# Performance work log

Measured on AMD Instinct MI355X. Metric: run time of the kernel, lower is better.

## Reference

```python
import jax, jax.numpy as jnp
import numpy as np
import math

B, S, D, H, L, F = 32, 512, 512, 8, 4, 1024
TD = 4 * D  # time embedding dim
DH = D // H
SCALE = 1.0 / math.sqrt(DH)


def _ln(x, g, b):
    m = jnp.mean(x, -1, keepdims=True)
    v = jnp.var(x, -1, keepdims=True)
    return (x - m) * jax.lax.rsqrt(v + 1e-5) * g + b


def setup_inputs() -> dict:
    key = jax.random.key(0)
    ks = jax.random.split(key, 12)
    w = lambda k, shp: jax.random.normal(k, shp, dtype=jnp.float32) * 0.02
    return {
        "x": jax.random.normal(ks[0], (B, S, D), dtype=jnp.float32),
        "time": jax.random.uniform(ks[1], (B,), dtype=jnp.float32) * 1000.0,
        "time_w1": w(ks[2], (TD, D)), "time_b1": jnp.zeros((TD,), jnp.float32),
        "time_w2": w(ks[3], (TD, TD)), "time_b2": jnp.zeros((TD,), jnp.float32),
        "Wq": w(ks[4], (L, D, D)), "bq": jnp.zeros((L, D), jnp.float32),
        "Wk": w(ks[5], (L, D, D)), "bk": jnp.zeros((L, D), jnp.float32),
        "Wv": w(ks[6], (L, D, D)), "bv": jnp.zeros((L, D), jnp.float32),
        "Wo": w(ks[7], (L, D, D)), "bo": jnp.zeros((L, D), jnp.float32),
        "attn_g": jnp.ones((L, D), jnp.float32), "attn_b": jnp.zeros((L, D), jnp.float32),
        "ffn_g": jnp.ones((L, D), jnp.float32), "ffn_b": jnp.zeros((L, D), jnp.float32),
        "W1": w(ks[8], (L, 2 * F, D)), "b1": jnp.zeros((L, 2 * F), jnp.float32),
        "W2": w(ks[9], (L, D, F)), "b2": jnp.zeros((L, D), jnp.float32),
        "Wt": w(ks[10], (L, 4 * F, TD)), "bt": jnp.zeros((L, 4 * F), jnp.float32),
        "head_g": jnp.ones((D,), jnp.float32), "head_b": jnp.zeros((D,), jnp.float32),
        "Wh": w(ks[11], (D, D)), "bh": jnp.zeros((D,), jnp.float32),
    }


def _forward(x, time, time_w1, time_b1, time_w2, time_b2,
             Wq, bq, Wk, bk, Wv, bv, Wo, bo,
             attn_g, attn_b, ffn_g, ffn_b,
             W1, b1, W2, b2, Wt, bt,
             head_g, head_b, Wh, bh):
    Bsz = x.shape[0]
    # --- sinusoidal time embedding + time MLP ---
    half = D // 2
    freqs = jnp.exp(jnp.arange(half, dtype=jnp.float32) * (-math.log(10000.0) / (half - 1)))
    e = time[:, None] * freqs[None, :]
    temb = jnp.concatenate([jnp.sin(e), jnp.cos(e)], axis=-1)  # [B, D]
    temb = jax.nn.gelu(temb @ time_w1.T + time_b1, approximate=False) @ time_w2.T + time_b2  # [B, 4D]
    for i in range(L):
        # attention (prenorm; block 0 skips the norm since first_prenormalization=False)
        h = x if i == 0 else _ln(x, attn_g[i], attn_b[i])
        q = (h @ Wq[i].T + bq[i]).reshape(Bsz, S, H, DH)
        k = (h @ Wk[i].T + bk[i]).reshape(Bsz, S, H, DH)
        v = (h @ Wv[i].T + bv[i]).reshape(Bsz, S, H, DH)
        logits = jnp.einsum('bqhd,bkhd->bhqk', q, k) * SCALE
        probs = jax.nn.softmax(logits, axis=-1)
        o = jnp.einsum('bhqk,bkhd->bqhd', probs, v).reshape(Bsz, S, D)
        x = x + (o @ Wo[i].T + bo[i])
        # FFN with FiLM time conditioning and ReGLU activation
        h = _ln(x, ffn_g[i], ffn_b[i])
        h1 = h @ W1[i].T + b1[i]  # [B, S, 2F]
        tm = jax.nn.silu(temb) @ Wt[i].T + bt[i]  # [B, 4F]
        scale, shift = jnp.split(tm[:, None, :], 2, axis=-1)  # each [B, 1, 2F]
        h1 = h1 * (scale + 1.0) + shift
        a, g = jnp.split(h1, 2, axis=-1)  # ReGLU: a * relu(g)
        x = x + ((a * jax.nn.relu(g)) @ W2[i].T + b2[i])
    # head: last token -> LayerNorm -> ReLU -> Linear
    z = _ln(x[:, -1], head_g, head_b)
    return jax.nn.relu(z) @ Wh.T + bh


def reference(x, time, time_w1, time_b1, time_w2, time_b2,
              Wq, bq, Wk, bk, Wv, bv, Wo, bo,
              attn_g, attn_b, ffn_g, ffn_b,
              W1, b1, W2, b2, Wt, bt,
              head_g, head_b, Wh, bh):
    return _forward(x, time, time_w1, time_b1, time_w2, time_b2,
                    Wq, bq, Wk, bk, Wv, bv, Wo, bo,
                    attn_g, attn_b, ffn_g, ffn_b,
                    W1, b1, W2, b2, Wt, bt,
                    head_g, head_b, Wh, bh)
```

## Files before the change

### kernel.cpp

```cpp
#include <hip/hip_runtime.h>
#include <math.h>

typedef __bf16 bf16_t;
typedef __bf16 bf16x8 __attribute__((ext_vector_type(8)));
typedef float f32x4 __attribute__((ext_vector_type(4)));

__device__ __forceinline__ void gload_lds16(const void* g, void* l) {
    __builtin_amdgcn_global_load_lds(
        (const __attribute__((address_space(1))) void*)g,
        (__attribute__((address_space(3))) void*)l, 16, 0, 0);
}

__global__ void k_f2b(const float* __restrict__ in, bf16_t* __restrict__ out, int n8) {
    int idx = blockIdx.x * 256 + threadIdx.x;
    if (idx >= n8) return;
    const float* p = in + (size_t)idx * 8;
    bf16x8 r;
#pragma unroll
    for (int j = 0; j < 8; j++) r[j] = (bf16_t)p[j];
    *(bf16x8*)(out + (size_t)idx * 8) = r;
}

__global__ void k_time_embed(const float* __restrict__ time, float* __restrict__ temb0) {
    int b = blockIdx.x;
    int j = threadIdx.x;
    float f = __expf((float)j * -0.036118981458730134f);
    float e = time[b] * f;
    temb0[(size_t)b * 512 + j] = sinf(e);
    temb0[(size_t)b * 512 + 256 + j] = cosf(e);
}

template<bool DO_NORM>
__global__ void k_ln(const float* __restrict__ x, const float* __restrict__ g,
                     const float* __restrict__ b, bf16_t* __restrict__ out) {
    int row = blockIdx.x * 4 + (threadIdx.x >> 6);
    int lane = threadIdx.x & 63;
    const float* xr = x + (size_t)row * 512 + lane * 8;
    float4 v0 = *(const float4*)xr;
    float4 v1 = *(const float4*)(xr + 4);
    float vals[8] = {v0.x, v0.y, v0.z, v0.w, v1.x, v1.y, v1.z, v1.w};
    bf16x8 r;
    if (DO_NORM) {
        float s = 0.f, sq = 0.f;
#pragma unroll
        for (int j = 0; j < 8; j++) { s += vals[j]; sq += vals[j] * vals[j]; }
#pragma unroll
        for (int m = 1; m < 64; m <<= 1) { s += __shfl_xor(s, m, 64); sq += __shfl_xor(sq, m, 64); }
        float mean = s * (1.0f / 512.0f);
        float var = sq * (1.0f / 512.0f) - mean * mean;
        float rstd = rsqrtf(var + 1e-5f);
        float4 g0 = *(const float4*)(g + lane * 8);
        float4 g1 = *(const float4*)(g + lane * 8 + 4);
        float4 b0 = *(const float4*)(b + lane * 8);
        float4 b1 = *(const float4*)(b + lane * 8 + 4);
        float gs[8] = {g0.x, g0.y, g0.z, g0.w, g1.x, g1.y, g1.z, g1.w};
        float bs[8] = {b0.x, b0.y, b0.z, b0.w, b1.x, b1.y, b1.z, b1.w};
#pragma unroll
        for (int j = 0; j < 8; j++) r[j] = (bf16_t)((vals[j] - mean) * rstd * gs[j] + bs[j]);
    } else {
#pragma unroll
        for (int j = 0; j < 8; j++) r[j] = (bf16_t)vals[j];
    }
    *(bf16x8*)(out + (size_t)row * 512 + lane * 8) = r;
}

__global__ void k_head_prep(const float* __restrict__ x, const float* __restrict__ g,
                            const float* __restrict__ b, float* __restrict__ z) {
    int row = blockIdx.x * 4 + (threadIdx.x >> 6);
    int lane = threadIdx.x & 63;
    const float* xr = x + ((size_t)row * 512 + 511) * 512 + lane * 8;
    float4 v0 = *(const float4*)xr;
    float4 v1 = *(const float4*)(xr + 4);
    float vals[8] = {v0.x, v0.y, v0.z, v0.w, v1.x, v1.y, v1.z, v1.w};
    float s = 0.f, sq = 0.f;
#pragma unroll
    for (int j = 0; j < 8; j++) { s += vals[j]; sq += vals[j] * vals[j]; }
#pragma unroll
    for (int m = 1; m < 64; m <<= 1) { s += __shfl_xor(s, m, 64); sq += __shfl_xor(sq, m, 64); }
    float mean = s * (1.0f / 512.0f);
    float var = sq * (1.0f / 512.0f) - mean * mean;
    float rstd = rsqrtf(var + 1e-5f);
    float o[8];
#pragma unroll
    for (int j = 0; j < 8; j++) {
        float gv = g[lane * 8 + j], bv = b[lane * 8 + j];
        o[j] = fmaxf((vals[j] - mean) * rstd * gv + bv, 0.0f);
    }
    float* zr = z + (size_t)row * 512 + lane * 8;
    *(float4*)zr = make_float4(o[0], o[1], o[2], o[3]);
    *(float4*)(zr + 4) = make_float4(o[4], o[5], o[6], o[7]);
}

template<int ACT>
__global__ __launch_bounds__(256)
void k_gemm32(const float* __restrict__ A, const float* __restrict__ W,
              const float* __restrict__ bias, float* __restrict__ out,
              int N, int K) {
    __shared__ float Asm[32 * 516];
    int tid = threadIdx.x;
    int n0 = blockIdx.x * 32;
    int nl = tid >> 3;
    int bq = tid & 7;
    float acc[4] = {0.f, 0.f, 0.f, 0.f};
    for (int k0 = 0; k0 < K; k0 += 512) {
        __syncthreads();
#pragma unroll
        for (int i = 0; i < 16; i++) {
            int fi = tid + i * 256;
            int row = fi >> 7;
            int cc = (fi & 127) << 2;
            *(float4*)&Asm[row * 516 + cc] = *(const float4*)&A[(size_t)row * K + k0 + cc];
        }
        __syncthreads();
        const float* Wr = W + (size_t)(n0 + nl) * K + k0;
        for (int kk = 0; kk < 512; kk += 4) {
            float4 w4 = *(const float4*)(Wr + kk);
#pragma unroll
            for (int j = 0; j < 4; j++) {
                float4 a4 = *(const float4*)&Asm[(bq + j * 8) * 516 + kk];
                acc[j] += a4.x * w4.x + a4.y * w4.y + a4.z * w4.z + a4.w * w4.w;
            }
        }
    }
#pragma unroll
    for (int j = 0; j < 4; j++) {
        float v = acc[j] + bias[n0 + nl];
        if (ACT == 1) v = 0.5f * v * (1.0f + erff(v * 0.70710678118654752f));
        if (ACT == 2) v = v / (1.0f + __expf(-v));
        out[(size_t)(bq + j * 8) * N + n0 + nl] = v;
    }
}

enum { EPI_QKV = 0, EPI_RESID = 1, EPI_FILMGLU = 2 };

template<int EPI, int K>
__global__ __launch_bounds__(256, 4)
void k_gemm_bt(const bf16_t* __restrict__ A, const bf16_t* __restrict__ W,
               const float* __restrict__ bias, const float* __restrict__ bias2,
               const float* __restrict__ bias3,
               void* __restrict__ out0, void* __restrict__ out1, void* __restrict__ out2,
               const float* __restrict__ tm) {
    __shared__ __align__(16) bf16_t Abuf[128 * 64];
    __shared__ __align__(16) bf16_t Bbuf[128 * 64];
    const int tid = threadIdx.x;
    const int bx = blockIdx.x, by = blockIdx.y;
    const int m0 = bx * 128;
    const int lane = tid & 63;
    const int wave = tid >> 6;
    const int wr = (wave >> 1) * 64, wc = (wave & 1) * 64;

    const int srow = tid >> 3;
    const int goff = ((tid & 7) * 16) ^ ((srow & 7) << 4);
    const char* Ag = (const char*)A;
    const char* Wg = (const char*)W;
    char* AbL = (char*)Abuf + tid * 16;
    char* BbL = (char*)Bbuf + tid * 16;
    int growB[4];
#pragma unroll
    for (int i = 0; i < 4; i++) {
        int r = srow + i * 32;
        if (EPI == EPI_FILMGLU) {
            int half = (r >> 5) & 1;
            int base = by * 64 + (r >> 6) * 32 + (r & 31);
            growB[i] = half * 1024 + base;
        } else {
            growB[i] = by * 128 + r;
        }
    }

    f32x4 acc[4][4] = {};
    for (int k0 = 0; k0 < K * 2; k0 += 128) {
        __syncthreads();
#pragma unroll
        for (int i = 0; i < 4; i++) {
            gload_lds16(Ag + (size_t)(m0 + srow + i * 32) * (K * 2) + k0 + goff, AbL + i * 4096);
            gload_lds16(Wg + (size_t)growB[i] * (K * 2) + k0 + goff, BbL + i * 4096);
        }
        __syncthreads();
#pragma unroll
        for (int kk = 0; kk < 2; kk++) {
            bf16x8 af[4], bfr[4];
#pragma unroll
            for (int i = 0; i < 4; i++) {
                int ar = wr + i * 16 + (lane & 15);
                af[i] = *(const bf16x8*)((const char*)Abuf + ar * 128 +
                         ((kk * 64 + (lane >> 4) * 16) ^ ((ar & 7) << 4)));
                int br = wc + i * 16 + (lane & 15);
                bfr[i] = *(const bf16x8*)((const char*)Bbuf + br * 128 +
                         ((kk * 64 + (lane >> 4) * 16) ^ ((br & 7) << 4)));
            }
#pragma unroll
            for (int i = 0; i < 4; i++)
#pragma unroll
                for (int j = 0; j < 4; j++)
                    acc[i][j] = __builtin_amdgcn_mfma_f32_16x16x32_bf16(af[i], bfr[j], acc[i][j], 0, 0, 0);
        }
    }

    const int b = m0 >> 9;
    if (EPI == EPI_QKV) {
        const int which = by >> 2;
        bf16_t* op = (bf16_t*)(which == 0 ? out0 : which == 1 ? out1 : out2);
        const float* bp = which == 0 ? bias : which == 1 ? bias2 : bias3;
#pragma unroll
        for (int i = 0; i < 4; i++) {
#pragma unroll
            for (int r = 0; r < 4; r++) {
                int s = (m0 + wr + i * 16 + (lane >> 4) * 4 + r) & 511;
#pragma unroll
                for (int j = 0; j < 4; j++) {
                    int c = (by & 3) * 128 + wc + j * 16 + (lane & 15);
                    float v = acc[i][j][r] + bp[c];
                    int h = c >> 6, dh = c & 63;
                    op[(((size_t)b * 8 + h) * 512 + s) * 64 + dh] = (bf16_t)v;
                }
            }
        }
    } else if (EPI == EPI_RESID) {
        float* op = (float*)out0;
#pragma unroll
        for (int i = 0; i < 4; i++) {
#pragma unroll
            for (int r = 0; r < 4; r++) {
                int row = m0 + wr + i * 16 + (lane >> 4) * 4 + r;
#pragma unroll
                for (int j = 0; j < 4; j++) {
                    int col = by * 128 + wc + j * 16 + (lane & 15);
                    op[(size_t)row * 512 + col] += acc[i][j][r] + bias[col];
                }
            }
        }
    } else {
        bf16_t* op = (bf16_t*)out0;
        const float* tml = tm + (size_t)b * 16384;
#pragma unroll
        for (int i = 0; i < 4; i++) {
#pragma unroll
            for (int r = 0; r < 4; r++) {
                int row = m0 + wr + i * 16 + (lane >> 4) * 4 + r;
#pragma unroll
                for (int jj = 0; jj < 2; jj++) {
                    int colA = by * 64 + (wave & 1) * 32 + jj * 16 + (lane & 15);
                    float av = acc[i][jj][r] + bias[colA];
                    float gv = acc[i][jj + 2][r] + bias[1024 + colA];
                    av = av * (1.0f + tml[colA]) + tml[2048 + colA];
                    gv = gv * (1.0f + tml[1024 + colA]) + tml[3072 + colA];
                    op[(size_t)row * 1024 + colA] = (bf16_t)(av * fmaxf(gv, 0.0f));
                }
            }
        }
    }
}

__global__ __launch_bounds__(256, 2)
void k_attn(const bf16_t* __restrict__ q, const bf16_t* __restrict__ k,
            const bf16_t* __restrict__ v, bf16_t* __restrict__ o) {
    __shared__ bf16_t q_lds[64][72];
    __shared__ bf16_t k_lds[64][72];
    __shared__ bf16_t vt_lds[64][72];
    __shared__ bf16_t p_lds[64][72];
    const int tid = threadIdx.x;
    const int lane = tid & 63;
    const int wave = tid >> 6;
    const int qt = blockIdx.x;
    const int bh = blockIdx.y;
    const bf16_t* qb = q + ((size_t)bh * 512 + qt * 64) * 64;
    const bf16_t* kb = k + (size_t)bh * 512 * 64;
    const bf16_t* vb = v + (size_t)bh * 512 * 64;
    const int sr = tid >> 2;
    const int sc = (tid & 3) * 16;
    {
        bf16x8 a0 = *(const bf16x8*)(qb + sr * 64 + sc);
        bf16x8 a1 = *(const bf16x8*)(qb + sr * 64 + sc + 8);
        bf16x8 ra, rb;
#pragma unroll
        for (int j = 0; j < 8; j++) {
            ra[j] = (bf16_t)((float)a0[j] * 0.125f);
            rb[j] = (bf16_t)((float)a1[j] * 0.125f);
        }
        *(bf16x8*)&q_lds[sr][sc] = ra;
        *(bf16x8*)&q_lds[sr][sc + 8] = rb;
    }
    float mrow[4], lrow[4];
    f32x4 oacc[4] = {};
#pragma unroll
    for (int r = 0; r < 4; r++) { mrow[r] = -1e30f; lrow[r] = 0.f; }
    for (int kt = 0; kt < 8; kt++) {
        __syncthreads();
        {
            const bf16_t* ks = kb + ((size_t)kt * 64 + sr) * 64 + sc;
            const bf16_t* vs = vb + ((size_t)kt * 64 + sr) * 64 + sc;
            *(bf16x8*)&k_lds[sr][sc] = *(const bf16x8*)ks;
            *(bf16x8*)&k_lds[sr][sc + 8] = *(const bf16x8*)(ks + 8);
            bf16x8 v0 = *(const bf16x8*)vs;
            bf16x8 v1 = *(const bf16x8*)(vs + 8);
#pragma unroll
            for (int j = 0; j < 8; j++) {
                vt_lds[sc + j][sr] = v0[j];
                vt_lds[sc + 8 + j][sr] = v1[j];
            }
        }
        __syncthreads();
        f32x4 sacc[4] = {};
#pragma unroll
        for (int kk = 0; kk < 2; kk++) {
            bf16x8 aq = *(const bf16x8*)&q_lds[wave * 16 + (lane & 15)][kk * 32 + (lane >> 4) * 8];
#pragma unroll
            for (int c = 0; c < 4; c++) {
                bf16x8 bk8 = *(const bf16x8*)&k_lds[c * 16 + (lane & 15)][kk * 32 + (lane >> 4) * 8];
                sacc[c] = __builtin_amdgcn_mfma_f32_16x16x32_bf16(aq, bk8, sacc[c], 0, 0, 0);
            }
        }
#pragma unroll
        for (int r = 0; r < 4; r++) {
            float mx = fmaxf(fmaxf(sacc[0][r], sacc[1][r]), fmaxf(sacc[2][r], sacc[3][r]));
#pragma unroll
            for (int m = 1; m < 16; m <<= 1) mx = fmaxf(mx, __shfl_xor(mx, m, 64));
            float newm = fmaxf(mrow[r], mx);
            float fsc = __expf(mrow[r] - newm);
            mrow[r] = newm;
            float p0 = __expf(sacc[0][r] - newm);
            float p1 = __expf(sacc[1][r] - newm);
            float p2 = __expf(sacc[2][r] - newm);
            float p3 = __expf(sacc[3][r] - newm);
            float ps = p0 + p1 + p2 + p3;
#pragma unroll
            for (int m = 1; m < 16; m <<= 1) ps += __shfl_xor(ps, m, 64);
            lrow[r] = lrow[r] * fsc + ps;
#pragma unroll
            for (int c = 0; c < 4; c++) oacc[c][r] *= fsc;
            int qrow = wave * 16 + (lane >> 4) * 4 + r;
            p_lds[qrow][(lane & 15)] = (bf16_t)p0;
            p_lds[qrow][16 + (lane & 15)] = (bf16_t)p1;
            p_lds[qrow][32 + (lane & 15)] = (bf16_t)p2;
            p_lds[qrow][48 + (lane & 15)] = (bf16_t)p3;
        }
        __syncthreads();
#pragma unroll
        for (int kk = 0; kk < 2; kk++) {
            bf16x8 ap = *(const bf16x8*)&p_lds[wave * 16 + (lane & 15)][kk * 32 + (lane >> 4) * 8];
#pragma unroll
            for (int c = 0; c < 4; c++) {
                bf16x8 bv8 = *(const bf16x8*)&vt_lds[c * 16 + (lane & 15)][kk * 32 + (lane >> 4) * 8];
                oacc[c] = __builtin_amdgcn_mfma_f32_16x16x32_bf16(ap, bv8, oacc[c], 0, 0, 0);
            }
        }
    }
    const int b = bh >> 3, h = bh & 7;
#pragma unroll
    for (int r = 0; r < 4; r++) {
        int s = qt * 64 + wave * 16 + (lane >> 4) * 4 + r;
        float inv = 1.0f / lrow[r];
#pragma unroll
        for (int c = 0; c < 4; c++) {
            o[((size_t)b * 512 + s) * 512 + h * 64 + c * 16 + (lane & 15)] = (bf16_t)(oacc[c][r] * inv);
        }
    }
}

extern "C" void kernel_launch(void* const* d_in, const int* in_sizes, int n_in,
                              void* d_out, int out_size, void* d_ws, size_t ws_size,
                              hipStream_t stream) {
    const float* x_in   = (const float*)d_in[0];
    const float* time_in= (const float*)d_in[1];
    const float* tw1    = (const float*)d_in[2];
    const float* tb1    = (const float*)d_in[3];
    const float* tw2    = (const float*)d_in[4];
    const float* tb2    = (const float*)d_in[5];
    const float* Wq     = (const float*)d_in[6];
    const float* bq     = (const float*)d_in[7];
    const float* Wk     = (const float*)d_in[8];
    const float* bk     = (const float*)d_in[9];
    const float* Wv     = (const float*)d_in[10];
    const float* bv     = (const float*)d_in[11];
    const float* Wo     = (const float*)d_in[12];
    const float* bo     = (const float*)d_in[13];
    const float* attn_g = (const float*)d_in[14];
    const float* attn_b = (const float*)d_in[15];
    const float* ffn_g  = (const float*)d_in[16];
    const float* ffn_b  = (const float*)d_in[17];
    const float* W1     = (const float*)d_in[18];
    const float* b1     = (const float*)d_in[19];
    const float* W2     = (const float*)d_in[20];
    const float* b2     = (const float*)d_in[21];
    const float* Wt     = (const float*)d_in[22];
    const float* bt     = (const float*)d_in[23];
    const float* head_g = (const float*)d_in[24];
    const float* head_b = (const float*)d_in[25];
    const float* Wh     = (const float*)d_in[26];
    const float* bh     = (const float*)d_in[27];

    size_t off = 0;
    auto alloc = [&](size_t bytes) {
        void* r = (char*)d_ws + off;
        off += (bytes + 255) & ~(size_t)255;
        return r;
    };
    bf16_t* wqkv_b = (bf16_t*)alloc((size_t)4 * 3 * 512 * 512 * 2);
    bf16_t* wo_b   = (bf16_t*)alloc((size_t)4 * 512 * 512 * 2);
    bf16_t* w1_b   = (bf16_t*)alloc((size_t)4 * 2048 * 512 * 2);
    bf16_t* w2_b   = (bf16_t*)alloc((size_t)4 * 512 * 1024 * 2);
    float*  x_ws   = (float*)alloc((size_t)16384 * 512 * 4);
    bf16_t* h_b    = (bf16_t*)alloc((size_t)16384 * 512 * 2);
    bf16_t* q_b    = (bf16_t*)alloc((size_t)16384 * 512 * 2);
    bf16_t* k_b    = (bf16_t*)alloc((size_t)16384 * 512 * 2);
    bf16_t* v_b    = (bf16_t*)alloc((size_t)16384 * 512 * 2);
    bf16_t* o_b    = (bf16_t*)alloc((size_t)16384 * 512 * 2);
    bf16_t* act_b  = (bf16_t*)alloc((size_t)16384 * 1024 * 2);
    float*  temb0  = (float*)alloc((size_t)32 * 512 * 4);
    float*  t1     = (float*)alloc((size_t)32 * 2048 * 4);
    float*  t2s    = (float*)alloc((size_t)32 * 2048 * 4);
    float*  tm_all = (float*)alloc((size_t)32 * 16384 * 4);
    float*  z      = (float*)alloc((size_t)32 * 512 * 4);

    for (int l = 0; l < 4; l++) {
        k_f2b<<<128, 256, 0, stream>>>(Wq + (size_t)l * 262144, wqkv_b + ((size_t)l * 3 + 0) * 262144, 32768);
        k_f2b<<<128, 256, 0, stream>>>(Wk + (size_t)l * 262144, wqkv_b + ((size_t)l * 3 + 1) * 262144, 32768);
        k_f2b<<<128, 256, 0, stream>>>(Wv + (size_t)l * 262144, wqkv_b + ((size_t)l * 3 + 2) * 262144, 32768);
    }
    k_f2b<<<512, 256, 0, stream>>>(Wo, wo_b, 131072);
    k_f2b<<<2048, 256, 0, stream>>>(W1, w1_b, 524288);
    k_f2b<<<1024, 256, 0, stream>>>(W2, w2_b, 262144);

    hipMemcpyAsync(x_ws, x_in, (size_t)16384 * 512 * 4, hipMemcpyDeviceToDevice, stream);

    k_time_embed<<<32, 256, 0, stream>>>(time_in, temb0);
    k_gemm32<1><<<64, 256, 0, stream>>>(temb0, tw1, tb1, t1, 2048, 512);
    k_gemm32<2><<<64, 256, 0, stream>>>(t1, tw2, tb2, t2s, 2048, 2048);
    k_gemm32<0><<<512, 256, 0, stream>>>(t2s, Wt, bt, tm_all, 16384, 2048);

    for (int l = 0; l < 4; l++) {
        if (l == 0)
            k_ln<false><<<4096, 256, 0, stream>>>(x_ws, nullptr, nullptr, h_b);
        else
            k_ln<true><<<4096, 256, 0, stream>>>(x_ws, attn_g + l * 512, attn_b + l * 512, h_b);

        k_gemm_bt<EPI_QKV, 512><<<dim3(128, 12), 256, 0, stream>>>(
            h_b, wqkv_b + (size_t)l * 786432,
            bq + l * 512, bk + l * 512, bv + l * 512,
            q_b, k_b, v_b, nullptr);

        k_attn<<<dim3(8, 256), 256, 0, stream>>>(q_b, k_b, v_b, o_b);

        k_gemm_bt<EPI_RESID, 512><<<dim3(128, 4), 256, 0, stream>>>(
            o_b, wo_b + (size_t)l * 262144,
            bo + l * 512, nullptr, nullptr,
            x_ws, nullptr, nullptr, nullptr);

        k_ln<true><<<4096, 256, 0, stream>>>(x_ws, ffn_g + l * 512, ffn_b + l * 512, h_b);

        k_gemm_bt<EPI_FILMGLU, 512><<<dim3(128, 16), 256, 0, stream>>>(
            h_b, w1_b + (size_t)l * 1048576,
            b1 + l * 2048, nullptr, nullptr,
            act_b, nullptr, nullptr, tm_all + l * 4096);

        k_gemm_bt<EPI_RESID, 1024><<<dim3(128, 4), 256, 0, stream>>>(
            act_b, w2_b + (size_t)l * 524288,
            b2 + l * 512, nullptr, nullptr,
            x_ws, nullptr, nullptr, nullptr);
    }

    k_head_prep<<<8, 256, 0, stream>>>(x_ws, head_g, head_b, z);
    k_gemm32<0><<<16, 256, 0, stream>>>(z, Wh, bh, (float*)d_out, 512, 512);
}
```

Before: 1.140 ms.

## Rework small-batch time GEMMs with register tiling and drop residual input copy

Replaces the small M=32 fp32 GEMM used for the time MLP, the FiLM projection and the head. The new kernel has each thread hold a 4x8 accumulator tile and split K across 8 lanes that are reduced with shuffles. This gives more reuse of each W load, which matters most for the large 16384x2048 Wt projection. It also removes the 32 MB device-to-device copy of x: layer 0 now reads x_in directly and the first residual GEMM writes x_in plus its delta into x_ws. The trade-off is higher register use per thread and extra shuffle-reduction work.

```diff
diff --git a/kernel.cpp b/kernel.cpp
--- a/kernel.cpp
+++ b/kernel.cpp
@@ -91,43 +91,60 @@
     *(float4*)(zr + 4) = make_float4(o[4], o[5], o[6], o[7]);
 }
 
-template<int ACT>
-__global__ __launch_bounds__(256)
-void k_gemm32(const float* __restrict__ A, const float* __restrict__ W,
-              const float* __restrict__ bias, float* __restrict__ out,
-              int N, int K) {
-    __shared__ float Asm[32 * 516];
-    int tid = threadIdx.x;
-    int n0 = blockIdx.x * 32;
-    int nl = tid >> 3;
-    int bq = tid & 7;
-    float acc[4] = {0.f, 0.f, 0.f, 0.f};
+template<int ACT, int K>
+__global__ __launch_bounds__(256, 2)
+void k_gemm_tm(const float* __restrict__ A, const float* __restrict__ W,
+               const float* __restrict__ bias, float* __restrict__ out, int N) {
+    __shared__ float Asm[32][516];
+    const int t = threadIdx.x;
+    const int kq = t & 7, rw = (t >> 3) & 7, bh = t >> 6;
+    const int n0 = blockIdx.x * 32;
+    float acc[4][8] = {};
     for (int k0 = 0; k0 < K; k0 += 512) {
         __syncthreads();
 #pragma unroll
         for (int i = 0; i < 16; i++) {
-            int fi = tid + i * 256;
-            int row = fi >> 7;
-            int cc = (fi & 127) << 2;
-            *(float4*)&Asm[row * 516 + cc] = *(const float4*)&A[(size_t)row * K + k0 + cc];
-        }
-        __syncthreads();
-        const float* Wr = W + (size_t)(n0 + nl) * K + k0;
-        for (int kk = 0; kk < 512; kk += 4) {
-            float4 w4 = *(const float4*)(Wr + kk);
-#pragma unroll
-            for (int j = 0; j < 4; j++) {
-                float4 a4 = *(const float4*)&Asm[(bq + j * 8) * 516 + kk];
-                acc[j] += a4.x * w4.x + a4.y * w4.y + a4.z * w4.z + a4.w * w4.w;
-            }
-        }
-    }
-#pragma unroll
-    for (int j = 0; j < 4; j++) {
-        float v = acc[j] + bias[n0 + nl];
-        if (ACT == 1) v = 0.5f * v * (1.0f + erff(v * 0.70710678118654752f));
-        if (ACT == 2) v = v / (1.0f + __expf(-v));
-        out[(size_t)(bq + j * 8) * N + n0 + nl] = v;
+            int fid = t + i * 256;
+            int row = fid >> 7, cc = (fid & 127) << 2;
+            *(float4*)&Asm[row][cc] = *(const float4*)&A[(size_t)row * K + k0 + cc];
+        }
+        __syncthreads();
+#pragma unroll 4
+        for (int j = 0; j < 16; j++) {
+            int kk = kq * 4 + j * 32;
+            float4 w4[4];
+#pragma unroll
+            for (int r = 0; r < 4; r++)
+                w4[r] = *(const float4*)&W[(size_t)(n0 + rw + r * 8) * K + k0 + kk];
+#pragma unroll
+            for (int b = 0; b < 8; b++) {
+                float4 a4 = *(const float4*)&Asm[bh * 8 + b][kk];
+#pragma unroll
+                for (int r = 0; r < 4; r++)
+                    acc[r][b] += a4.x * w4[r].x + a4.y * w4[r].y + a4.z * w4[r].z + a4.w * w4[r].w;
+            }
+        }
+    }
+#pragma unroll
+    for (int m = 1; m < 8; m <<= 1)
+#pragma unroll
+        for (int r = 0; r < 4; r++)
+#pragma unroll
+            for (int b = 0; b < 8; b++)
+                acc[r][b] += __shfl_xor(acc[r][b], m, 64);
+    if (kq == 0) {
+#pragma unroll
+        for (int r = 0; r < 4; r++) {
+            int n = n0 + rw + r * 8;
+            float bv = bias[n];
+#pragma unroll
+            for (int b = 0; b < 8; b++) {
+                float v = acc[r][b] + bv;
+                if (ACT == 1) v = 0.5f * v * (1.0f + erff(v * 0.70710678118654752f));
+                if (ACT == 2) v = v / (1.0f + __expf(-v));
+                out[(size_t)(bh * 8 + b) * N + n] = v;
+            }
+        }
     }
 }
 
@@ -218,6 +235,7 @@
         }
     } else if (EPI == EPI_RESID) {
         float* op = (float*)out0;
+        const float* rs = (const float*)out1;
 #pragma unroll
         for (int i = 0; i < 4; i++) {
 #pragma unroll
@@ -226,7 +244,8 @@
 #pragma unroll
                 for (int j = 0; j < 4; j++) {
                     int col = by * 128 + wc + j * 16 + (lane & 15);
-                    op[(size_t)row * 512 + col] += acc[i][j][r] + bias[col];
+                    size_t idx = (size_t)row * 512 + col;
+                    op[idx] = rs[idx] + acc[i][j][r] + bias[col];
                 }
             }
         }
@@ -422,16 +441,14 @@
     k_f2b<<<2048, 256, 0, stream>>>(W1, w1_b, 524288);
     k_f2b<<<1024, 256, 0, stream>>>(W2, w2_b, 262144);
 
-    hipMemcpyAsync(x_ws, x_in, (size_t)16384 * 512 * 4, hipMemcpyDeviceToDevice, stream);
-
     k_time_embed<<<32, 256, 0, stream>>>(time_in, temb0);
-    k_gemm32<1><<<64, 256, 0, stream>>>(temb0, tw1, tb1, t1, 2048, 512);
-    k_gemm32<2><<<64, 256, 0, stream>>>(t1, tw2, tb2, t2s, 2048, 2048);
-    k_gemm32<0><<<512, 256, 0, stream>>>(t2s, Wt, bt, tm_all, 16384, 2048);
+    k_gemm_tm<1, 512><<<64, 256, 0, stream>>>(temb0, tw1, tb1, t1, 2048);
+    k_gemm_tm<2, 2048><<<64, 256, 0, stream>>>(t1, tw2, tb2, t2s, 2048);
+    k_gemm_tm<0, 2048><<<512, 256, 0, stream>>>(t2s, Wt, bt, tm_all, 16384);
 
     for (int l = 0; l < 4; l++) {
         if (l == 0)
-            k_ln<false><<<4096, 256, 0, stream>>>(x_ws, nullptr, nullptr, h_b);
+            k_ln<false><<<4096, 256, 0, stream>>>(x_in, nullptr, nullptr, h_b);
         else
             k_ln<true><<<4096, 256, 0, stream>>>(x_ws, attn_g + l * 512, attn_b + l * 512, h_b);
 
@@ -445,7 +462,7 @@
         k_gemm_bt<EPI_RESID, 512><<<dim3(128, 4), 256, 0, stream>>>(
             o_b, wo_b + (size_t)l * 262144,
             bo + l * 512, nullptr, nullptr,
-            x_ws, nullptr, nullptr, nullptr);
+            x_ws, (void*)(l == 0 ? x_in : x_ws), nullptr, nullptr);
 
         k_ln<true><<<4096, 256, 0, stream>>>(x_ws, ffn_g + l * 512, ffn_b + l * 512, h_b);
 
@@ -457,9 +474,9 @@
         k_gemm_bt<EPI_RESID, 1024><<<dim3(128, 4), 256, 0, stream>>>(
             act_b, w2_b + (size_t)l * 524288,
             b2 + l * 512, nullptr, nullptr,
-            x_ws, nullptr, nullptr, nullptr);
+            x_ws, x_ws, nullptr, nullptr);
     }
 
     k_head_prep<<<8, 256, 0, stream>>>(x_ws, head_g, head_b, z);
-    k_gemm32<0><<<16, 256, 0, stream>>>(z, Wh, bh, (float*)d_out, 512, 512);
-}
+    k_gemm_tm<0, 512><<<16, 256, 0, stream>>>(z, Wh, bh, (float*)d_out, 512);
+}
```

Measured after the change: 1.178 ms. +3.3%, slower.
